# Performance work log

Hardware: AMD Instinct MI355X
Metric: run time of the kernel (lower is better)

The kernel has to match this reference:

```python
import jax, jax.numpy as jnp
import numpy as np
from jax import lax

D = 1024      # embed_dim
L = 8         # num_blocks
H = 8         # num_heads
P = 4         # patch_size
IMG = 64
B = 64
N = (IMG // P) ** 2 + 1   # 257 tokens (cls + patches)
DF = 4 * D
EPS = 1e-6


def _ln(x, g, b):
    m = jnp.mean(x, axis=-1, keepdims=True)
    v = jnp.var(x, axis=-1, keepdims=True)
    return (x - m) * jax.lax.rsqrt(v + EPS) * g + b


def setup_inputs() -> dict:
    key = jax.random.key(0)
    ks = jax.random.split(key, 20)
    s = 0.02
    return {
        "x": jax.random.normal(ks[0], (B, IMG, IMG, 3), jnp.float32),
        "conv_w": jax.random.normal(ks[1], (P, P, 3, D), jnp.float32) * s,
        "conv_b": jnp.zeros((D,), jnp.float32),
        "cls_token": jax.random.normal(ks[2], (1, 1, D), jnp.float32) * s,
        "pos_emb": jax.random.normal(ks[3], (N, D), jnp.float32) * s,
        "ln1_g": jnp.ones((L, D), jnp.float32),
        "ln1_b": jnp.zeros((L, D), jnp.float32),
        "wq": jax.random.normal(ks[4], (L, D, D), jnp.float32) * s,
        "wk": jax.random.normal(ks[5], (L, D, D), jnp.float32) * s,
        "wv": jax.random.normal(ks[6], (L, D, D), jnp.float32) * s,
        "proj_w": jax.random.normal(ks[7], (L, D, D), jnp.float32) * s,
        "proj_b": jnp.zeros((L, D), jnp.float32),
        "ln2_g": jnp.ones((L, D), jnp.float32),
        "ln2_b": jnp.zeros((L, D), jnp.float32),
        "mlp1_w": jax.random.normal(ks[8], (L, D, DF), jnp.float32) * s,
        "mlp1_b": jnp.zeros((L, DF), jnp.float32),
        "mlp2_w": jax.random.normal(ks[9], (L, DF, D), jnp.float32) * s,
        "mlp2_b": jnp.zeros((L, D), jnp.float32),
    }


def _forward(x, conv_w, conv_b, cls_token, pos_emb, ln1_g, ln1_b, wq, wk, wv,
             proj_w, proj_b, ln2_g, ln2_b, mlp1_w, mlp1_b, mlp2_w, mlp2_b):
    bsz = x.shape[0]
    # patch embedding: strided conv, NHWC / HWIO
    r = lax.conv_general_dilated(x, conv_w, (P, P), 'VALID',
                                 dimension_numbers=('NHWC', 'HWIO', 'NHWC')) + conv_b
    tokens = r.reshape(bsz, -1, D)                         # [B, 256, D]
    cls = jnp.broadcast_to(cls_token, (bsz, 1, D))
    t = jnp.concatenate([cls, tokens], axis=1) + pos_emb[None]   # [B, N, D]

    hd = D // H
    scale = hd ** -0.5
    for i in range(L):
        xn = _ln(t, ln1_g[i], ln1_b[i])
        q = (xn @ wq[i] * scale).reshape(bsz, N, H, hd)
        k = (xn @ wk[i]).reshape(bsz, N, H, hd)
        v = (xn @ wv[i]).reshape(bsz, N, H, hd)
        attn = jax.nn.softmax(jnp.einsum('bqhd,bkhd->bhqk', q, k), axis=-1)
        y = jnp.einsum('bhqk,bkhd->bqhd', attn, v).reshape(bsz, N, D)
        t = t + y @ proj_w[i] + proj_b[i]
        xn2 = _ln(t, ln2_g[i], ln2_b[i])
        h = jax.nn.gelu(xn2 @ mlp1_w[i] + mlp1_b[i], approximate=False)
        t = t + h @ mlp2_w[i] + mlp2_b[i]
    return t[:, 0]   # gp='none' -> cls token


def reference(x, conv_w, conv_b, cls_token, pos_emb, ln1_g, ln1_b, wq, wk, wv,
              proj_w, proj_b, ln2_g, ln2_b, mlp1_w, mlp1_b, mlp2_w, mlp2_b):
    return _forward(x, conv_w, conv_b, cls_token, pos_emb, ln1_g, ln1_b, wq, wk, wv,
                    proj_w, proj_b, ln2_g, ln2_b, mlp1_w, mlp1_b, mlp2_w, mlp2_b)
```

## Files before the change

### kernel.cpp

```cpp
#include <hip/hip_runtime.h>
#include <math.h>

typedef __bf16 bf16;
typedef __bf16 bf16x8 __attribute__((ext_vector_type(8)));
typedef __bf16 bf16x2v __attribute__((ext_vector_type(2)));
typedef float f32x4 __attribute__((ext_vector_type(4)));

#define DD     1024
#define NL     8
#define NTOK   257
#define NB     64
#define DFF    4096
#define MM     (NB*NTOK)
#define NP     288
#define HD     128
#define CHUNK  128

__device__ __forceinline__ void gld16(const void* g, void* l) {
  __builtin_amdgcn_global_load_lds((__attribute__((address_space(1))) void*)g,
                                   (__attribute__((address_space(3))) void*)l,
                                   16, 0, 0);
}

template<int NT, int NR>
__device__ __forceinline__ void stage_sw(const bf16* __restrict__ p, int ld,
                                         int row0, int rmax, int k0,
                                         char* lds, int t) {
  int wb = (t >> 6) << 10;
  int cs = ((((t & 3) - (t >> 3)) & 3) << 3);
  #pragma unroll
  for (int i = 0; i < (NR*4)/NT; ++i) {
    int r = row0 + i*(NT/4) + (t >> 2);
    r = r < rmax ? r : rmax;
    gld16(p + (long)r*ld + k0 + cs, lds + i*(NT*16) + wb);
  }
}

__device__ __forceinline__ void swz_xy(int& X, int& Y) {
  int gx = gridDim.x, gy = gridDim.y;
  int G = gx * gy;
  int orig = blockIdx.y * gx + blockIdx.x;
  int q = G >> 3, r = G & 7;
  int xcd = orig & 7, j = orig >> 3;
  int wg = (xcd < r ? xcd*(q+1) : r*(q+1) + (xcd-r)*q) + j;
  X = wg / gy; Y = wg - (wg / gy) * gy;
}

__device__ __forceinline__ void frag_mfma(const char* cA, const char* cB,
                                          int wr, int wc, int ro, int soff,
                                          f32x4 acc[4][4]) {
  bf16x8 af[4], bfr[4];
  #pragma unroll
  for (int i = 0; i < 4; ++i)
    af[i]  = *(const bf16x8*)(cA + (wr + i*16 + ro)*64 + soff);
  #pragma unroll
  for (int j = 0; j < 4; ++j)
    bfr[j] = *(const bf16x8*)(cB + (wc + j*16 + ro)*64 + soff);
  #pragma unroll
  for (int i = 0; i < 4; ++i)
    #pragma unroll
    for (int j = 0; j < 4; ++j)
      acc[i][j] = __builtin_amdgcn_mfma_f32_16x16x32_bf16(af[i], bfr[j], acc[i][j], 0, 0, 0);
}

template<int NT, int BN>
__device__ __forceinline__ void gemm_core(const bf16* __restrict__ A, int lda, int ar0, int armax,
                                          const bf16* __restrict__ Bt, int ldb, int br0, int brmax,
                                          int K, f32x4 acc[4][4], char* lds) {
  int t = threadIdx.x;
  int lane = t & 63, w = t >> 6;
  int wr = (NT == 256 ? (w >> 1) : (w >> 2)) << 6;
  int wc = (NT == 256 ? (w & 1)  : (w & 3))  << 6;
  int ro = lane & 15, q = lane >> 4;
  int soff = ((q + (ro >> 1)) & 3) << 4;
  constexpr int AB = 128*64;
  constexpr int BB = BN*64;
  char* lB = lds + 2*AB;

  stage_sw<NT,128>(A,  lda, ar0, armax, 0, lds, t);
  stage_sw<NT,BN> (Bt, ldb, br0, brmax, 0, lB,  t);
  __syncthreads();
  int cur = 0;
  for (int k0 = 32; k0 < K; k0 += 32) {
    stage_sw<NT,128>(A,  lda, ar0, armax, k0, lds + (cur^1)*AB, t);
    stage_sw<NT,BN> (Bt, ldb, br0, brmax, k0, lB  + (cur^1)*BB, t);
    frag_mfma(lds + cur*AB, lB + cur*BB, wr, wc, ro, soff, acc);
    __syncthreads();
    cur ^= 1;
  }
  frag_mfma(lds + cur*AB, lB + cur*BB, wr, wc, ro, soff, acc);
}

#define ACC_INIT f32x4 acc[4][4]; { f32x4 z = {0.f,0.f,0.f,0.f}; \
  for (int i=0;i<4;i++) for (int j=0;j<4;j++) acc[i][j]=z; }

#define EPILOG_IDX(NT) int te = threadIdx.x; int lane_ = te & 63; int w_ = te >> 6; \
  int r0 = ((NT==256 ? (w_>>1) : (w_>>2)) << 6) + ((lane_ >> 4) << 2); \
  int c0 = ((NT==256 ? (w_&1)  : (w_&3))  << 6) + (lane_ & 15);

__global__ void __launch_bounds__(512) k_gemm_qkv(const bf16* __restrict__ A,
    const bf16* __restrict__ Bt, bf16* __restrict__ qb, bf16* __restrict__ kb,
    bf16* __restrict__ vT) {
  __shared__ char lds[2*8192 + 2*16384];
  int X, Y; swz_xy(X, Y);
  ACC_INIT;
  gemm_core<512,256>(A, DD, X*128, MM-1, Bt, DD, Y*256, 3071, DD, acc, lds);
  EPILOG_IDX(512);
  int mb = X*128, nb = Y*256;
  #pragma unroll
  for (int i=0;i<4;i++)
    #pragma unroll
    for (int r=0;r<4;r++) {
      int m = mb + r0 + i*16 + r;
      if (m < MM) {
        unsigned bb = (unsigned)m / NTOK;
        int tok = m - (int)bb*NTOK;
        #pragma unroll
        for (int j=0;j<4;j++) {
          int n = nb + c0 + j*16;
          bf16 val = (bf16)acc[i][j][r];
          if (n < 2048) {
            (n < 1024 ? qb : kb)[(long)m*DD + (n & 1023)] = val;
          } else {
            int nv = n - 2048, h = nv >> 7, d = nv & 127;
            vT[(((long)(bb*8+h))*HD + d)*NP + tok] = val;
          }
        }
      }
    }
}

__global__ void __launch_bounds__(512) k_gemm_resid(const bf16* __restrict__ A,
    const bf16* __restrict__ Bt, const float* __restrict__ bias,
    float* __restrict__ T, int K) {
  __shared__ char lds[2*8192 + 2*16384];
  int X, Y; swz_xy(X, Y);
  ACC_INIT;
  gemm_core<512,256>(A, K, X*128, MM-1, Bt, K, Y*256, 1023, K, acc, lds);
  EPILOG_IDX(512);
  int mb = X*128, nb = Y*256;
  #pragma unroll
  for (int i=0;i<4;i++)
    #pragma unroll
    for (int r=0;r<4;r++) {
      int m = mb + r0 + i*16 + r;
      if (m < MM) {
        #pragma unroll
        for (int j=0;j<4;j++) {
          int n = nb + c0 + j*16;
          long idx = (long)m*DD + n;
          T[idx] = T[idx] + acc[i][j][r] + bias[n];
        }
      }
    }
}

__global__ void __launch_bounds__(512) k_gemm_gelu(const bf16* __restrict__ A,
    const bf16* __restrict__ Bt, const float* __restrict__ bias,
    bf16* __restrict__ Hb) {
  __shared__ char lds[2*8192 + 2*16384];
  int X, Y; swz_xy(X, Y);
  ACC_INIT;
  gemm_core<512,256>(A, DD, X*128, MM-1, Bt, DD, Y*256, 4095, DD, acc, lds);
  EPILOG_IDX(512);
  int mb = X*128, nb = Y*256;
  #pragma unroll
  for (int i=0;i<4;i++)
    #pragma unroll
    for (int r=0;r<4;r++) {
      int m = mb + r0 + i*16 + r;
      if (m < MM) {
        #pragma unroll
        for (int j=0;j<4;j++) {
          int n = nb + c0 + j*16;
          float vv = acc[i][j][r] + bias[n];
          float ge = 0.5f*vv*(1.f + erff(vv*0.70710678118654752f));
          Hb[(long)m*DFF + n] = (bf16)ge;
        }
      }
    }
}

__global__ void __launch_bounds__(256) k_attn_s(const bf16* __restrict__ q,
    const bf16* __restrict__ kk, bf16* __restrict__ P, int bh0) {
  __shared__ char lds[2*8192 + 2*8192];
  int l = blockIdx.z; int bh = bh0 + l; int b = bh >> 3; int h = bh & 7;
  const bf16* Ab = q  + (long)b*NTOK*DD + h*HD;
  const bf16* Bb = kk + (long)b*NTOK*DD + h*HD;
  ACC_INIT;
  gemm_core<256,128>(Ab, DD, blockIdx.x*128, NTOK-1, Bb, DD, blockIdx.y*128, NTOK-1, HD, acc, lds);
  EPILOG_IDX(256);
  bf16* Pp = P + (long)l*NP*NP;
  int mb = blockIdx.x*128, nb = blockIdx.y*128;
  #pragma unroll
  for (int i=0;i<4;i++)
    #pragma unroll
    for (int r=0;r<4;r++) {
      int m = mb + r0 + i*16 + r;
      if (m < NTOK) {
        #pragma unroll
        for (int j=0;j<4;j++) {
          int n = nb + c0 + j*16;
          if (n < NTOK) Pp[(long)m*NP + n] = (bf16)acc[i][j][r];
        }
      }
    }
}

__global__ void __launch_bounds__(256) k_attn_pv(const bf16* __restrict__ P,
    const bf16* __restrict__ vT, bf16* __restrict__ y, int bh0) {
  __shared__ char lds[2*8192 + 2*8192];
  int l = blockIdx.z; int bh = bh0 + l; int b = bh >> 3; int h = bh & 7;
  const bf16* Ab = P  + (long)l*NP*NP;
  const bf16* Bb = vT + (long)bh*HD*NP;
  ACC_INIT;
  gemm_core<256,128>(Ab, NP, blockIdx.x*128, NP-1, Bb, NP, 0, HD-1, NP, acc, lds);
  EPILOG_IDX(256);
  int mb = blockIdx.x*128;
  #pragma unroll
  for (int i=0;i<4;i++)
    #pragma unroll
    for (int r=0;r<4;r++) {
      int m = mb + r0 + i*16 + r;
      if (m < NTOK) {
        #pragma unroll
        for (int j=0;j<4;j++) {
          int n = c0 + j*16;
          y[((long)b*NTOK + m)*DD + h*HD + n] = (bf16)acc[i][j][r];
        }
      }
    }
}

__global__ void __launch_bounds__(256) k_ln(const float* __restrict__ T,
    const float* __restrict__ g, const float* __restrict__ be,
    bf16* __restrict__ out) {
  int row = blockIdx.x;
  const float4* x4 = (const float4*)(T + (long)row*DD);
  int t = threadIdx.x;
  float4 v = x4[t];
  float s  = v.x+v.y+v.z+v.w;
  float ss = v.x*v.x+v.y*v.y+v.z*v.z+v.w*v.w;
  #pragma unroll
  for (int o=32;o;o>>=1){ s += __shfl_down(s,o); ss += __shfl_down(ss,o); }
  __shared__ float rsum[4], rsq[4];
  int lane = t&63, w = t>>6;
  if (lane==0){ rsum[w]=s; rsq[w]=ss; }
  __syncthreads();
  float S  = rsum[0]+rsum[1]+rsum[2]+rsum[3];
  float SS = rsq[0]+rsq[1]+rsq[2]+rsq[3];
  float mean = S*(1.f/DD);
  float var  = SS*(1.f/DD) - mean*mean;
  float rs = rsqrtf(var + 1e-6f);
  float4 gg = ((const float4*)g)[t];
  float4 bb = ((const float4*)be)[t];
  bf16* o = out + (long)row*DD + t*4;
  o[0]=(bf16)((v.x-mean)*rs*gg.x+bb.x);
  o[1]=(bf16)((v.y-mean)*rs*gg.y+bb.y);
  o[2]=(bf16)((v.z-mean)*rs*gg.z+bb.z);
  o[3]=(bf16)((v.w-mean)*rs*gg.w+bb.w);
}

__global__ void __launch_bounds__(256) k_softmax(bf16* __restrict__ P) {
  int t = threadIdx.x, lane = t & 63, w = t >> 6;
  int row = blockIdx.x*4 + w;
  int l = row / NTOK, qq = row - l*NTOK;
  bf16* p = P + (long)l*NP*NP + (long)qq*NP;
  float v[5]; float mx = -1e30f;
  #pragma unroll
  for (int i=0;i<5;i++){
    int c = lane + i*64;
    v[i] = (c < NTOK) ? (float)p[c] : -1e30f;
    mx = fmaxf(mx, v[i]);
  }
  #pragma unroll
  for (int o=32;o;o>>=1) mx = fmaxf(mx, __shfl_xor(mx, o));
  float s = 0.f;
  #pragma unroll
  for (int i=0;i<5;i++){ v[i] = __expf(v[i]-mx); s += v[i]; }
  #pragma unroll
  for (int o=32;o;o>>=1) s += __shfl_xor(s, o);
  float inv = 1.f / s;
  #pragma unroll
  for (int i=0;i<5;i++){ int c = lane + i*64; if (c < NTOK) p[c] = (bf16)(v[i]*inv); }
  if (lane < NP-NTOK) p[NTOK+lane] = (bf16)0.f;
}

__global__ void __launch_bounds__(256) k_transpose64(const float* __restrict__ in,
    bf16* __restrict__ out, int R, int C, float scale) {
  __shared__ float tile[64][65];
  int c0 = blockIdx.x*64, r0 = blockIdx.y*64;
  int t = threadIdx.x;
  int tr = t >> 5, tc = (t & 31) * 2;
  #pragma unroll
  for (int i = 0; i < 8; ++i) {
    int r = r0 + tr + i*8;
    float2 v = *(const float2*)&in[(long)r*C + c0 + tc];
    tile[tr + i*8][tc] = v.x; tile[tr + i*8][tc+1] = v.y;
  }
  __syncthreads();
  #pragma unroll
  for (int i = 0; i < 8; ++i) {
    int c = c0 + tr + i*8;
    bf16x2v o;
    o.x = (bf16)(tile[tc  ][tr + i*8] * scale);
    o.y = (bf16)(tile[tc+1][tr + i*8] * scale);
    *(bf16x2v*)&out[(long)c*R + r0 + tc] = o;
  }
}

__global__ void __launch_bounds__(256) k_embed(const float* __restrict__ x,
    const float* __restrict__ cw, const float* __restrict__ cb,
    const float* __restrict__ cls, const float* __restrict__ pos,
    float* __restrict__ T) {
  int blk = blockIdx.x; int b = blk / NTOK, tok = blk - b*NTOK;
  long orow = (long)(b*NTOK + tok)*DD;
  int t = threadIdx.x;
  if (tok == 0) {
    #pragma unroll
    for (int i=0;i<4;i++){ int d=t+i*256; T[orow+d] = cls[d] + pos[d]; }
    return;
  }
  __shared__ float patch[48];
  int pi = tok-1, py = pi>>4, px = pi&15;
  if (t < 48) {
    int i = t/12, j = (t/3)&3, c = t%3;
    patch[t] = x[(((long)(b*64 + py*4 + i))*64 + px*4 + j)*3 + c];
  }
  __syncthreads();
  float a[4];
  #pragma unroll
  for (int i=0;i<4;i++) a[i] = cb[t+i*256];
  for (int p=0;p<48;p++){
    float pv = patch[p];
    const float* wrow = cw + p*DD;
    #pragma unroll
    for (int i=0;i<4;i++) a[i] += pv * wrow[t+i*256];
  }
  #pragma unroll
  for (int i=0;i<4;i++){ int d=t+i*256; T[orow+d] = a[i] + pos[(long)tok*DD+d]; }
}

__global__ void __launch_bounds__(256) k_out(const float* __restrict__ T,
                                             float* __restrict__ out) {
  int b = blockIdx.x, t = threadIdx.x;
  #pragma unroll
  for (int i=0;i<4;i++){
    int d = t + i*256;
    out[(long)b*DD + d] = T[(long)b*NTOK*DD + d];
  }
}

extern "C" void kernel_launch(void* const* d_in, const int* in_sizes, int n_in,
                              void* d_out, int out_size, void* d_ws, size_t ws_size,
                              hipStream_t stream) {
  const float* x      = (const float*)d_in[0];
  const float* conv_w = (const float*)d_in[1];
  const float* conv_b = (const float*)d_in[2];
  const float* cls    = (const float*)d_in[3];
  const float* pos    = (const float*)d_in[4];
  const float* ln1_g  = (const float*)d_in[5];
  const float* ln1_b  = (const float*)d_in[6];
  const float* wq     = (const float*)d_in[7];
  const float* wk     = (const float*)d_in[8];
  const float* wv     = (const float*)d_in[9];
  const float* proj_w = (const float*)d_in[10];
  const float* proj_b = (const float*)d_in[11];
  const float* ln2_g  = (const float*)d_in[12];
  const float* ln2_b  = (const float*)d_in[13];
  const float* mlp1_w = (const float*)d_in[14];
  const float* mlp1_b = (const float*)d_in[15];
  const float* mlp2_w = (const float*)d_in[16];
  const float* mlp2_b = (const float*)d_in[17];

  const size_t TBUF_OFF = 0;
  const size_t XN_OFF   = 67371008;
  const size_t C_OFF    = XN_OFF + 33685504;
  const size_t NEED     = C_OFF + 151519232;
  if (ws_size < NEED) return;

  char* base = (char*)d_ws;
  float* tbuf  = (float*)(base + TBUF_OFF);
  bf16*  xn    = (bf16*)(base + XN_OFF);
  char*  C     = base + C_OFF;
  bf16* wqkvT  = (bf16*)(C + 0);
  bf16* projT  = wqkvT;
  bf16* qb     = (bf16*)(C + 6291456);
  bf16* kb     = (bf16*)(C + 39976960);
  bf16* vT     = (bf16*)(C + 73662464);
  bf16* Pc     = (bf16*)(C + 111411200);
  bf16* m1T    = (bf16*)(C + 0);
  bf16* m2T    = (bf16*)(C + 8388608);
  bf16* hb     = (bf16*)(C + 16777216);

  const float qscale = 0.08838834764831845f;

  k_embed<<<MM, 256, 0, stream>>>(x, conv_w, conv_b, cls, pos, tbuf);

  for (int i = 0; i < NL; ++i) {
    const long wo = (long)i*DD*DD;
    k_transpose64<<<dim3(16,16), 256, 0, stream>>>(wq + wo, wqkvT,             DD, DD, qscale);
    k_transpose64<<<dim3(16,16), 256, 0, stream>>>(wk + wo, wqkvT + 1024*1024, DD, DD, 1.f);
    k_transpose64<<<dim3(16,16), 256, 0, stream>>>(wv + wo, wqkvT + 2*1024*1024, DD, DD, 1.f);
    k_ln<<<MM, 256, 0, stream>>>(tbuf, ln1_g + i*DD, ln1_b + i*DD, xn);
    k_gemm_qkv<<<dim3(129,12), 512, 0, stream>>>(xn, wqkvT, qb, kb, vT);
    k_transpose64<<<dim3(16,16), 256, 0, stream>>>(proj_w + wo, projT, DD, DD, 1.f);
    for (int c = 0; c < 512/CHUNK; ++c) {
      k_attn_s <<<dim3(3,3,CHUNK), 256, 0, stream>>>(qb, kb, Pc, c*CHUNK);
      k_softmax<<<(CHUNK*NTOK)/4, 256, 0, stream>>>(Pc);
      k_attn_pv<<<dim3(3,1,CHUNK), 256, 0, stream>>>(Pc, vT, xn, c*CHUNK);
    }
    k_gemm_resid<<<dim3(129,4), 512, 0, stream>>>(xn, projT, proj_b + i*DD, tbuf, DD);
    k_ln<<<MM, 256, 0, stream>>>(tbuf, ln2_g + i*DD, ln2_b + i*DD, xn);
    k_transpose64<<<dim3(64,16), 256, 0, stream>>>(mlp1_w + (long)i*DD*DFF, m1T, DD, DFF, 1.f);
    k_transpose64<<<dim3(16,64), 256, 0, stream>>>(mlp2_w + (long)i*DFF*DD, m2T, DFF, DD, 1.f);
    k_gemm_gelu <<<dim3(129,16), 512, 0, stream>>>(xn, m1T, mlp1_b + i*DFF, hb);
    k_gemm_resid<<<dim3(129,4),  512, 0, stream>>>(hb, m2T, mlp2_b + i*DD, tbuf, DFF);
  }

  k_out<<<NB, 256, 0, stream>>>(tbuf, (float*)d_out);
}
```

Measured before the change: 7.272 ms.

## Use 256x256 GEMM tiles with a 4-stage direct-to-LDS pipeline

Replaces the shared GEMM core with a new 256x256 output tile per 512-thread block, where each wave accumulates 8x4 MFMA fragments. Tiles are staged through a four-deep LDS ring filled by global_load_lds, using explicit vmcnt waits, raw barriers and s_setprio around the MFMA block. Grid rows are halved to match. The aim is more data reuse per loaded byte and better hiding of global-load latency. In exchange it needs 128KB of LDS and more accumulator registers per thread, which limits occupancy.

```diff
diff --git a/kernel.cpp b/kernel.cpp
--- a/kernel.cpp
+++ b/kernel.cpp
@@ -98,17 +98,85 @@
   int r0 = ((NT==256 ? (w_>>1) : (w_>>2)) << 6) + ((lane_ >> 4) << 2); \
   int c0 = ((NT==256 ? (w_&1)  : (w_&3))  << 6) + (lane_ & 15);
 
-__global__ void __launch_bounds__(512) k_gemm_qkv(const bf16* __restrict__ A,
+__device__ __forceinline__ void gemm_core256(const bf16* __restrict__ A, int lda, int ar0, int armax,
+                                             const bf16* __restrict__ Bt, int ldb, int br0, int brmax,
+                                             int K, f32x4 acc[8][4], char* lds) {
+  int t = threadIdx.x;
+  int lane = t & 63, w = t >> 6;
+  int wr = (w >> 2) << 7;
+  int wc = (w & 3) << 6;
+  int ro = lane & 15, q = lane >> 4;
+  int soff = ((q + (ro >> 1)) & 3) << 4;
+  int wb = w << 10;
+  int cs = ((((t & 3) - (t >> 3)) & 3) << 3);
+
+  const bf16 *pA0, *pA1, *pB0, *pB1;
+  {
+    int r;
+    r = ar0 + (t >> 2);       r = r < armax ? r : armax;  pA0 = A  + (long)r*lda + cs;
+    r = ar0 + 128 + (t >> 2); r = r < armax ? r : armax;  pA1 = A  + (long)r*lda + cs;
+    r = br0 + (t >> 2);       r = r < brmax ? r : brmax;  pB0 = Bt + (long)r*ldb + cs;
+    r = br0 + 128 + (t >> 2); r = r < brmax ? r : brmax;  pB1 = Bt + (long)r*ldb + cs;
+  }
+
+  int nk = K >> 5;
+  auto stage = [&](int ks) {
+    char* sA = lds + ((ks & 3) << 15);
+    char* sB = sA + 16384;
+    int k0 = ks << 5;
+    gld16(pA0 + k0, sA + wb);
+    gld16(pA1 + k0, sA + 8192 + wb);
+    gld16(pB0 + k0, sB + wb);
+    gld16(pB1 + k0, sB + 8192 + wb);
+  };
+
+  stage(0); stage(1); stage(2);
+  for (int ks = 0; ks < nk; ++ks) {
+    int rem = nk - 1 - ks;
+    if (rem >= 2)      asm volatile("s_waitcnt vmcnt(8)" ::: "memory");
+    else if (rem == 1) asm volatile("s_waitcnt vmcnt(4)" ::: "memory");
+    else               asm volatile("s_waitcnt vmcnt(0)" ::: "memory");
+    __builtin_amdgcn_sched_barrier(0);
+    __builtin_amdgcn_s_barrier();
+    __builtin_amdgcn_sched_barrier(0);
+    if (ks + 3 < nk) stage(ks + 3);
+    char* sA = lds + ((ks & 3) << 15);
+    char* sB = sA + 16384;
+    bf16x8 af[8], bfr[4];
+    #pragma unroll
+    for (int i = 0; i < 8; ++i)
+      af[i]  = *(const bf16x8*)(sA + (wr + i*16 + ro)*64 + soff);
+    #pragma unroll
+    for (int j = 0; j < 4; ++j)
+      bfr[j] = *(const bf16x8*)(sB + (wc + j*16 + ro)*64 + soff);
+    __builtin_amdgcn_s_setprio(1);
+    #pragma unroll
+    for (int i = 0; i < 8; ++i)
+      #pragma unroll
+      for (int j = 0; j < 4; ++j)
+        acc[i][j] = __builtin_amdgcn_mfma_f32_16x16x32_bf16(af[i], bfr[j], acc[i][j], 0, 0, 0);
+    __builtin_amdgcn_s_setprio(0);
+  }
+}
+
+#define ACC_INIT256 f32x4 acc[8][4]; { f32x4 z = {0.f,0.f,0.f,0.f}; \
+  for (int i=0;i<8;i++) for (int j=0;j<4;j++) acc[i][j]=z; }
+
+#define EPILOG_IDX256 int te = threadIdx.x; int lane_ = te & 63; int w_ = te >> 6; \
+  int r0 = ((w_ >> 2) << 7) + ((lane_ >> 4) << 2); \
+  int c0 = ((w_ & 3) << 6) + (lane_ & 15);
+
+__global__ void __launch_bounds__(512, 2) k_gemm_qkv(const bf16* __restrict__ A,
     const bf16* __restrict__ Bt, bf16* __restrict__ qb, bf16* __restrict__ kb,
     bf16* __restrict__ vT) {
-  __shared__ char lds[2*8192 + 2*16384];
+  __shared__ char lds[131072];
   int X, Y; swz_xy(X, Y);
-  ACC_INIT;
-  gemm_core<512,256>(A, DD, X*128, MM-1, Bt, DD, Y*256, 3071, DD, acc, lds);
-  EPILOG_IDX(512);
-  int mb = X*128, nb = Y*256;
-  #pragma unroll
-  for (int i=0;i<4;i++)
+  ACC_INIT256;
+  gemm_core256(A, DD, X*256, MM-1, Bt, DD, Y*256, 3071, DD, acc, lds);
+  EPILOG_IDX256;
+  int mb = X*256, nb = Y*256;
+  #pragma unroll
+  for (int i=0;i<8;i++)
     #pragma unroll
     for (int r=0;r<4;r++) {
       int m = mb + r0 + i*16 + r;
@@ -130,17 +198,17 @@
     }
 }
 
-__global__ void __launch_bounds__(512) k_gemm_resid(const bf16* __restrict__ A,
+__global__ void __launch_bounds__(512, 2) k_gemm_resid(const bf16* __restrict__ A,
     const bf16* __restrict__ Bt, const float* __restrict__ bias,
     float* __restrict__ T, int K) {
-  __shared__ char lds[2*8192 + 2*16384];
+  __shared__ char lds[131072];
   int X, Y; swz_xy(X, Y);
-  ACC_INIT;
-  gemm_core<512,256>(A, K, X*128, MM-1, Bt, K, Y*256, 1023, K, acc, lds);
-  EPILOG_IDX(512);
-  int mb = X*128, nb = Y*256;
-  #pragma unroll
-  for (int i=0;i<4;i++)
+  ACC_INIT256;
+  gemm_core256(A, K, X*256, MM-1, Bt, K, Y*256, 1023, K, acc, lds);
+  EPILOG_IDX256;
+  int mb = X*256, nb = Y*256;
+  #pragma unroll
+  for (int i=0;i<8;i++)
     #pragma unroll
     for (int r=0;r<4;r++) {
       int m = mb + r0 + i*16 + r;
@@ -155,17 +223,17 @@
     }
 }
 
-__global__ void __launch_bounds__(512) k_gemm_gelu(const bf16* __restrict__ A,
+__global__ void __launch_bounds__(512, 2) k_gemm_gelu(const bf16* __restrict__ A,
     const bf16* __restrict__ Bt, const float* __restrict__ bias,
     bf16* __restrict__ Hb) {
-  __shared__ char lds[2*8192 + 2*16384];
+  __shared__ char lds[131072];
   int X, Y; swz_xy(X, Y);
-  ACC_INIT;
-  gemm_core<512,256>(A, DD, X*128, MM-1, Bt, DD, Y*256, 4095, DD, acc, lds);
-  EPILOG_IDX(512);
-  int mb = X*128, nb = Y*256;
-  #pragma unroll
-  for (int i=0;i<4;i++)
+  ACC_INIT256;
+  gemm_core256(A, DD, X*256, MM-1, Bt, DD, Y*256, 4095, DD, acc, lds);
+  EPILOG_IDX256;
+  int mb = X*256, nb = Y*256;
+  #pragma unroll
+  for (int i=0;i<8;i++)
     #pragma unroll
     for (int r=0;r<4;r++) {
       int m = mb + r0 + i*16 + r;
@@ -403,19 +471,19 @@
     k_transpose64<<<dim3(16,16), 256, 0, stream>>>(wk + wo, wqkvT + 1024*1024, DD, DD, 1.f);
     k_transpose64<<<dim3(16,16), 256, 0, stream>>>(wv + wo, wqkvT + 2*1024*1024, DD, DD, 1.f);
     k_ln<<<MM, 256, 0, stream>>>(tbuf, ln1_g + i*DD, ln1_b + i*DD, xn);
-    k_gemm_qkv<<<dim3(129,12), 512, 0, stream>>>(xn, wqkvT, qb, kb, vT);
+    k_gemm_qkv<<<dim3(65,12), 512, 0, stream>>>(xn, wqkvT, qb, kb, vT);
     k_transpose64<<<dim3(16,16), 256, 0, stream>>>(proj_w + wo, projT, DD, DD, 1.f);
     for (int c = 0; c < 512/CHUNK; ++c) {
       k_attn_s <<<dim3(3,3,CHUNK), 256, 0, stream>>>(qb, kb, Pc, c*CHUNK);
       k_softmax<<<(CHUNK*NTOK)/4, 256, 0, stream>>>(Pc);
       k_attn_pv<<<dim3(3,1,CHUNK), 256, 0, stream>>>(Pc, vT, xn, c*CHUNK);
     }
-    k_gemm_resid<<<dim3(129,4), 512, 0, stream>>>(xn, projT, proj_b + i*DD, tbuf, DD);
+    k_gemm_resid<<<dim3(65,4), 512, 0, stream>>>(xn, projT, proj_b + i*DD, tbuf, DD);
     k_ln<<<MM, 256, 0, stream>>>(tbuf, ln2_g + i*DD, ln2_b + i*DD, xn);
     k_transpose64<<<dim3(64,16), 256, 0, stream>>>(mlp1_w + (long)i*DD*DFF, m1T, DD, DFF, 1.f);
     k_transpose64<<<dim3(16,64), 256, 0, stream>>>(mlp2_w + (long)i*DFF*DD, m2T, DFF, DD, 1.f);
-    k_gemm_gelu <<<dim3(129,16), 512, 0, stream>>>(xn, m1T, mlp1_b + i*DFF, hb);
-    k_gemm_resid<<<dim3(129,4),  512, 0, stream>>>(hb, m2T, mlp2_b + i*DD, tbuf, DFF);
+    k_gemm_gelu <<<dim3(65,16), 512, 0, stream>>>(xn, m1T, mlp1_b + i*DFF, hb);
+    k_gemm_resid<<<dim3(65,4),  512, 0, stream>>>(hb, m2T, mlp2_b + i*DD, tbuf, DFF);
   }
 
   k_out<<<NB, 256, 0, stream>>>(tbuf, (float*)d_out);
```

Measured after the change: 8.137 ms. 1.12x slower.
